# Kernel optimization log

Hardware: AMD Instinct MI355X
Metric: run time of the kernel (lower is better)

The kernel has to match this reference:

```python
import jax, jax.numpy as jnp
import numpy as np

B, S, HID = 4, 4096, 1024
H, D = 16, 64  # num_head, attn_dim
EPS = 1e-6


def setup_inputs() -> dict:
    key = jax.random.key(0)
    ks = jax.random.split(key, 9)
    sc = 1.0 / np.sqrt(HID)
    return {
        "x": jax.random.normal(ks[0], (B, S, HID), jnp.float32),
        "Wq": jax.random.normal(ks[1], (HID, H * D), jnp.float32) * sc,
        "bq": jnp.zeros((H * D,), jnp.float32),
        "Wk": jax.random.normal(ks[2], (HID, H * D), jnp.float32) * sc,
        "bk": jnp.zeros((H * D,), jnp.float32),
        "Wv": jax.random.normal(ks[3], (HID, H * D), jnp.float32) * sc,
        "bv": jnp.zeros((H * D,), jnp.float32),
        "Wo": jax.random.normal(ks[4], (H * D, HID), jnp.float32) * sc,
        "bo": jnp.zeros((HID,), jnp.float32),
    }


def _phi(x):
    # feature_map == 'elu': elu(x) + 1
    return jax.nn.elu(x) + 1.0


def reference(x, Wq, bq, Wk, bk, Wv, bv, Wo, bo):
    bs, n, _ = x.shape
    # projections -> [b, n, h, d], then scan axis first -> [n, b, h, d]
    Q = _phi((x @ Wq + bq).reshape(bs, n, H, D)).transpose(1, 0, 2, 3)
    K = _phi((x @ Wk + bk).reshape(bs, n, H, D)).transpose(1, 0, 2, 3)
    V = (x @ Wv + bv).reshape(bs, n, H, D).transpose(1, 0, 2, 3)

    KV0 = jnp.zeros((bs, H, D, D), x.dtype)
    Ks0 = jnp.zeros((bs, H, D), x.dtype)

    def step(carry, qkv):
        KV, Ks = carry
        qi, ki, vi = qkv  # each [b, h, d]
        KV = KV + jnp.einsum('bhd,bhe->bhde', ki, vi)
        Ks = Ks + ki
        num = jnp.einsum('bhd,bhde->bhe', qi, KV)
        den = jnp.einsum('bhd,bhd->bh', qi, Ks)
        return (KV, Ks), num / (den[..., None] + EPS)

    _, out = jax.lax.scan(step, (KV0, Ks0), (Q, K, V))  # out: [n, b, h, d]
    out = out.transpose(1, 0, 2, 3).reshape(bs, n, H * D)
    return out @ Wo + bo
```

## Files before the change

### kernel.cpp

```cpp
#include <hip/hip_runtime.h>
#include <stdint.h>


#define DEVI __device__ __forceinline__

typedef __attribute__((ext_vector_type(8))) short bf16x8;
typedef __attribute__((ext_vector_type(4))) float f32x4;
typedef unsigned short u16;

DEVI u16 f2bf(float f) {
  union { float f; uint32_t u; } x; x.f = f;
  return (u16)((x.u + 0x7FFFu + ((x.u >> 16) & 1u)) >> 16);
}
DEVI float bf2f(u16 u) {
  union { uint32_t u; float f; } x; x.u = ((uint32_t)u) << 16;
  return x.f;
}
DEVI f32x4 mfma16(bf16x8 a, bf16x8 b, f32x4 c) {
  return __builtin_amdgcn_mfma_f32_16x16x32_bf16(a, b, c, 0, 0, 0);
}

typedef __attribute__((address_space(3))) void* lds_vp;
typedef const __attribute__((address_space(1))) void* glb_vp;
DEVI void gload_lds16(const void* g, void* l) {
  __builtin_amdgcn_global_load_lds((glb_vp)g, (lds_vp)l, 16, 0, 0);
}

#define BAR()   asm volatile("s_barrier" ::: "memory")
#define LGKM0() do { asm volatile("s_waitcnt lgkmcnt(0)" ::: "memory"); \
                     __builtin_amdgcn_sched_barrier(0); } while (0)

static constexpr int Ss  = 4096;
static constexpr int Hh  = 16;
static constexpr int CC  = 64;
static constexpr int NCC = Ss / CC;

__global__ __launch_bounds__(256) void cvt_bf16_k(const float* __restrict__ in,
                                                  u16* __restrict__ out, int n8) {
  const int i = blockIdx.x * 256 + threadIdx.x;
  if (i >= n8) return;
  const float4* p = (const float4*)(in + (size_t)i * 8);
  const float4 a = p[0], b = p[1];
  union { uint4 v; u16 s[8]; } u;
  u.s[0] = f2bf(a.x); u.s[1] = f2bf(a.y); u.s[2] = f2bf(a.z); u.s[3] = f2bf(a.w);
  u.s[4] = f2bf(b.x); u.s[5] = f2bf(b.y); u.s[6] = f2bf(b.z); u.s[7] = f2bf(b.w);
  ((uint4*)out)[i] = u.v;
}

__global__ __launch_bounds__(256) void transpose_cvt4_k(const float* __restrict__ w0,
                                                        const float* __restrict__ w1,
                                                        const float* __restrict__ w2,
                                                        const float* __restrict__ w3,
                                                        u16* __restrict__ dqkv,
                                                        u16* __restrict__ dwo) {
  __shared__ float tl[32][33];
  const int z = blockIdx.z;
  const float* in = (z == 0) ? w0 : (z == 1) ? w1 : (z == 2) ? w2 : w3;
  u16* out = (z < 3) ? (dqkv + (size_t)z * 1024 * 1024) : dwo;
  const int tx = threadIdx.x & 31, ty = threadIdx.x >> 5;
  const int bx = blockIdx.x, by = blockIdx.y;
#pragma unroll
  for (int j = 0; j < 4; ++j)
    tl[ty + j * 8][tx] = in[(size_t)(by * 32 + ty + j * 8) * 1024 + bx * 32 + tx];
  __syncthreads();
#pragma unroll
  for (int j = 0; j < 4; ++j)
    out[(size_t)(bx * 32 + ty + j * 8) * 1024 + by * 32 + tx] = f2bf(tl[tx][ty + j * 8]);
}

template <bool FUSED, bool OUTF32>
__global__ __launch_bounds__(512, 2) void gemm256_k(const u16* __restrict__ A,
                                                    const u16* __restrict__ BT,
                                                    const float* __restrict__ b0,
                                                    const float* __restrict__ b1,
                                                    const float* __restrict__ b2,
                                                    void* __restrict__ out,
                                                    int M, int K) {
  __shared__ __attribute__((aligned(16))) u16 lds[65536];
  const int t = threadIdx.x, lane = t & 63, w = t >> 6;
  const int wm = w >> 2, wn = w & 3;

  const int nx = gridDim.x;
  const int nwg = nx * gridDim.y;
  const int bid = blockIdx.y * nx + blockIdx.x;
  const int swz = (bid & 7) * (nwg >> 3) + (bid >> 3);
  const int bx = swz % nx, by = swz / nx;
  const int m0 = by * 256, n0 = bx * 256;

  const u16* gA = A + (size_t)m0 * K;
  const u16* gB = BT + (size_t)n0 * K;

  const int sr = t >> 2;
  const int sc = (t & 3) ^ ((sr >> 1) & 3);
  auto stage = [&](const u16* gm, u16* dst, int kof) {
    gload_lds16(gm + (size_t)sr * K + kof + sc * 8, dst + t * 8);
    gload_lds16(gm + (size_t)(sr + 128) * K + kof + sc * 8, dst + 4096 + t * 8);
  };

  f32x4 acc[8][4];
#pragma unroll
  for (int i = 0; i < 8; ++i)
#pragma unroll
    for (int j = 0; j < 4; ++j) acc[i][j] = f32x4{0.f, 0.f, 0.f, 0.f};

  stage(gA, lds, 0);          stage(gB, lds + 32768, 0);
  stage(gA, lds + 8192, 32);  stage(gB, lds + 40960, 32);
  asm volatile("s_waitcnt vmcnt(4)" ::: "memory");
  BAR();

  const int fr = lane & 15, kq = lane >> 4;
  const int rdko = ((kq ^ ((fr >> 1) & 3)) << 3);
  const int arow0 = wm * 128 + fr;
  const int brow0 = wn * 64 + fr;

  const int nk = K >> 6;
  for (int kt = 0; kt < nk; ++kt) {
    const int d = kt & 1;
    const bool pf = (kt + 1 < nk);
    const int kon = (kt + 1) << 6;
    u16* Ac = lds + d * 16384;
    u16* Bc = lds + 32768 + d * 16384;
    u16* An = lds + (d ^ 1) * 16384;
    u16* Bn = lds + 32768 + (d ^ 1) * 16384;
    bf16x8 af[8], bg0, bg1;
#pragma unroll
    for (int h = 0; h < 2; ++h) {
      const u16* Ah = Ac + h * 8192;
      const u16* Bh = Bc + h * 8192;
#pragma unroll
      for (int fi = 0; fi < 8; ++fi)
        af[fi] = *(const bf16x8*)(Ah + (arow0 + fi * 16) * 32 + rdko);
      bg0 = *(const bf16x8*)(Bh + brow0 * 32 + rdko);
      bg1 = *(const bf16x8*)(Bh + (brow0 + 16) * 32 + rdko);
      if (pf) stage(gA, An + h * 8192, kon + h * 32);
      BAR();
      LGKM0();
      __builtin_amdgcn_s_setprio(1);
#pragma unroll
      for (int fi = 0; fi < 8; ++fi) {
        acc[fi][0] = mfma16(af[fi], bg0, acc[fi][0]);
        acc[fi][1] = mfma16(af[fi], bg1, acc[fi][1]);
      }
      __builtin_amdgcn_s_setprio(0);
      __builtin_amdgcn_sched_barrier(0);
      BAR();
      bg0 = *(const bf16x8*)(Bh + (brow0 + 32) * 32 + rdko);
      bg1 = *(const bf16x8*)(Bh + (brow0 + 48) * 32 + rdko);
      if (pf) stage(gB, Bn + h * 8192, kon + h * 32);
      BAR();
      LGKM0();
      __builtin_amdgcn_s_setprio(1);
#pragma unroll
      for (int fi = 0; fi < 8; ++fi) {
        acc[fi][2] = mfma16(af[fi], bg0, acc[fi][2]);
        acc[fi][3] = mfma16(af[fi], bg1, acc[fi][3]);
      }
      __builtin_amdgcn_s_setprio(0);
      __builtin_amdgcn_sched_barrier(0);
      if (h == 0) {
        if (pf) asm volatile("s_waitcnt vmcnt(4)" ::: "memory");
        else    asm volatile("s_waitcnt vmcnt(0)" ::: "memory");
      } else if (pf) {
        asm volatile("s_waitcnt vmcnt(4)" ::: "memory");
      }
      BAR();
    }
  }

  const int rowg = (lane >> 4) * 4;
  if constexpr (!OUTF32) {
    __syncthreads();
    const int seg  = FUSED ? (n0 >> 10) : 0;
    const int lcol0 = FUSED ? (n0 & 1023) : n0;
    const float* bp = b0;
    if constexpr (FUSED) bp = (seg == 0) ? b0 : (seg == 1) ? b1 : b2;
#pragma unroll
    for (int fj = 0; fj < 4; ++fj) {
      const int col = wn * 64 + fj * 16 + fr;
      const float bv = bp[lcol0 + col];
#pragma unroll
      for (int fi = 0; fi < 8; ++fi) {
#pragma unroll
        for (int rr = 0; rr < 4; ++rr) {
          const int row = wm * 128 + fi * 16 + rowg + rr;
          float v = acc[fi][fj][rr] + bv;
          if (FUSED && seg < 2) v = (v > 0.f) ? (v + 1.f) : __expf(v);
          lds[row * 256 + (((col >> 3) ^ ((row >> 2) & 31)) << 3) + (col & 7)] = f2bf(v);
        }
      }
    }
    __syncthreads();
    u16* outp = (u16*)out + (size_t)seg * M * 1024 + (size_t)m0 * 1024 + lcol0;
#pragma unroll
    for (int it = 0; it < 16; ++it) {
      const int g = it * 512 + t;
      const int row = g >> 5, c16 = g & 31;
      const uint4 v = *(const uint4*)&lds[row * 256 + ((c16 ^ ((row >> 2) & 31)) << 3)];
      *(uint4*)(outp + (size_t)row * 1024 + c16 * 8) = v;
    }
  } else {
    float* flds = (float*)lds;
#pragma unroll
    for (int pass = 0; pass < 2; ++pass) {
      __syncthreads();
      if (wm == pass) {
#pragma unroll
        for (int fj = 0; fj < 4; ++fj) {
          const int col = wn * 64 + fj * 16 + fr;
          const float bv = b0[n0 + col];
#pragma unroll
          for (int fi = 0; fi < 8; ++fi) {
#pragma unroll
            for (int rr = 0; rr < 4; ++rr) {
              const int rl = fi * 16 + rowg + rr;
              flds[rl * 256 + (((col >> 2) ^ ((rl >> 2) & 63)) << 2) + (col & 3)] =
                  acc[fi][fj][rr] + bv;
            }
          }
        }
      }
      __syncthreads();
      float* outp = (float*)out + (size_t)(m0 + pass * 128) * 1024 + n0;
#pragma unroll
      for (int it = 0; it < 16; ++it) {
        const int g = it * 512 + t;
        const int row = g >> 6, c16 = g & 63;
        const uint4 v = *(const uint4*)&flds[row * 256 + ((c16 ^ ((row >> 2) & 63)) << 2)];
        *(uint4*)(outp + (size_t)row * 1024 + c16 * 4) = v;
      }
    }
  }
}

__global__ __launch_bounds__(256) void chunk_kv_k(const u16* __restrict__ Kb,
                                                  const u16* __restrict__ Vb,
                                                  u16* __restrict__ KVTc,
                                                  float* __restrict__ Ksc) {
  const int c = blockIdx.x, h = blockIdx.y, b = blockIdx.z;
  __shared__ u16 KT[64][72], VT[64][72];
  const int t = threadIdx.x, lane = t & 63, w = t >> 6;
  {
    const int i = t >> 2, c0 = (t & 3) * 16;
    const size_t g = ((size_t)(b * Ss + c * CC + i)) * 1024 + h * 64 + c0;
    const u16* kp = Kb + g;
    const u16* vp = Vb + g;
#pragma unroll
    for (int j = 0; j < 16; ++j) { KT[c0 + j][i] = kp[j]; VT[c0 + j][i] = vp[j]; }
  }
  __syncthreads();
  f32x4 acc[4];
#pragma unroll
  for (int j = 0; j < 4; ++j) acc[j] = f32x4{0.f, 0.f, 0.f, 0.f};
  const int fr = lane & 15, kq = (lane >> 4) * 8;
#pragma unroll
  for (int kk = 0; kk < 2; ++kk) {
    const bf16x8 av = *(const bf16x8*)&VT[w * 16 + fr][kk * 32 + kq];
#pragma unroll
    for (int fj = 0; fj < 4; ++fj) {
      const bf16x8 bk = *(const bf16x8*)&KT[fj * 16 + fr][kk * 32 + kq];
      acc[fj] = mfma16(av, bk, acc[fj]);
    }
  }
  const size_t base = ((size_t)((b * Hh + h) * NCC + c)) * 4096;
#pragma unroll
  for (int fj = 0; fj < 4; ++fj)
#pragma unroll
    for (int rr = 0; rr < 4; ++rr) {
      const int e = w * 16 + (lane >> 4) * 4 + rr;
      const int d = fj * 16 + fr;
      KVTc[base + (size_t)e * 64 + d] = f2bf(acc[fj][rr]);
    }
  if (t < 64) {
    float s = 0.f;
#pragma unroll
    for (int ii = 0; ii < 8; ++ii) {
      const bf16x8 kv = *(const bf16x8*)&KT[t][ii * 8];
#pragma unroll
      for (int j = 0; j < 8; ++j) s += bf2f((u16)kv[j]);
    }
    Ksc[((size_t)((b * Hh + h) * NCC + c)) * 64 + t] = s;
  }
}

__global__ __launch_bounds__(256) void prefix_k(const u16* __restrict__ KVTc,
                                                const float* __restrict__ Ksc,
                                                u16* __restrict__ KVpreT,
                                                float* __restrict__ Kspre) {
  const int bh = blockIdx.x, eg = blockIdx.y;
  const int t = threadIdx.x;
  const int e4 = eg * 1024 + t * 4;
  const u16* src = KVTc + (size_t)bh * NCC * 4096 + e4;
  u16* dst = KVpreT + (size_t)bh * NCC * 4096 + e4;
  const float* kss = Ksc + (size_t)bh * NCC * 64 + t;
  float* ksd = Kspre + (size_t)bh * NCC * 64 + t;
  float run[4] = {0.f, 0.f, 0.f, 0.f};
  float rk = 0.f;
  for (int c = 0; c < NCC; ++c) {
    union { uint2 v; u16 s[4]; } in, ov;
    in.v = *(const uint2*)(src + (size_t)c * 4096);
#pragma unroll
    for (int j = 0; j < 4; ++j) { ov.s[j] = f2bf(run[j]); run[j] += bf2f(in.s[j]); }
    *(uint2*)(dst + (size_t)c * 4096) = ov.v;
    if (eg == 0 && t < 64) { ksd[(size_t)c * 64] = rk; rk += kss[(size_t)c * 64]; }
  }
}

__global__ __launch_bounds__(256) void chunk_out_k(const u16* __restrict__ Qb,
                                                   const u16* __restrict__ Kb,
                                                   const u16* __restrict__ Vb,
                                                   const u16* __restrict__ KVpreT,
                                                   const float* __restrict__ Kspre,
                                                   u16* __restrict__ attn) {
  const int c = blockIdx.x, h = blockIdx.y, b = blockIdx.z;
  const int bh = b * Hh + h;
  __shared__ u16 Ql[64][72], Kl[64][72], VT[64][72], Pl[64][72];
  __shared__ float den[64];
  const int t = threadIdx.x, lane = t & 63, w = t >> 6;

  {
    const int i = t >> 2, c0 = (t & 3) * 16;
    const size_t g = ((size_t)(b * Ss + c * CC + i)) * 1024 + h * 64 + c0;
    const uint4* qp = (const uint4*)(Qb + g);
    uint4* qd = (uint4*)&Ql[i][c0]; qd[0] = qp[0]; qd[1] = qp[1];
    const uint4* kp = (const uint4*)(Kb + g);
    uint4* kd = (uint4*)&Kl[i][c0]; kd[0] = kp[0]; kd[1] = kp[1];
    const u16* vp = Vb + g;
#pragma unroll
    for (int j = 0; j < 16; ++j) VT[c0 + j][i] = vp[j];
  }
  __syncthreads();

  f32x4 sacc[4];
#pragma unroll
  for (int fj = 0; fj < 4; ++fj) sacc[fj] = f32x4{0.f, 0.f, 0.f, 0.f};
#pragma unroll
  for (int kd = 0; kd < 2; ++kd) {
    const bf16x8 aq = *(const bf16x8*)&Ql[w * 16 + (lane & 15)][kd * 32 + (lane >> 4) * 8];
#pragma unroll
    for (int fj = 0; fj < 4; ++fj) {
      const bf16x8 bk = *(const bf16x8*)&Kl[fj * 16 + (lane & 15)][kd * 32 + (lane >> 4) * 8];
      sacc[fj] = mfma16(aq, bk, sacc[fj]);
    }
  }
  float rowsum[4] = {0.f, 0.f, 0.f, 0.f};
#pragma unroll
  for (int fj = 0; fj < 4; ++fj) {
#pragma unroll
    for (int rr = 0; rr < 4; ++rr) {
      const int i_loc = w * 16 + (lane >> 4) * 4 + rr;
      const int j_loc = fj * 16 + (lane & 15);
      const float v = (j_loc <= i_loc) ? sacc[fj][rr] : 0.f;
      Pl[i_loc][j_loc] = f2bf(v);
      rowsum[rr] += v;
    }
  }
#pragma unroll
  for (int off = 1; off < 16; off <<= 1) {
#pragma unroll
    for (int rr = 0; rr < 4; ++rr) rowsum[rr] += __shfl_xor(rowsum[rr], off, 64);
  }
  if ((lane & 15) == 0) {
#pragma unroll
    for (int rr = 0; rr < 4; ++rr) den[w * 16 + (lane >> 4) * 4 + rr] = rowsum[rr];
  }
  __syncthreads();
  {
    const int i = t >> 2, part = t & 3;
    const float* ksp = Kspre + ((size_t)(bh * NCC + c)) * 64 + part * 16;
    float s = 0.f;
#pragma unroll
    for (int sg = 0; sg < 2; ++sg) {
      const bf16x8 q = *(const bf16x8*)&Ql[i][part * 16 + sg * 8];
#pragma unroll
      for (int j = 0; j < 8; ++j) s += bf2f((u16)q[j]) * ksp[sg * 8 + j];
    }
    s += __shfl_xor(s, 1, 64);
    s += __shfl_xor(s, 2, 64);
    if (part == 0) den[i] = den[i] + s + 1e-6f;
  }
  __syncthreads();

  f32x4 oacc[4];
#pragma unroll
  for (int fj = 0; fj < 4; ++fj) oacc[fj] = f32x4{0.f, 0.f, 0.f, 0.f};
  const u16* kvb = KVpreT + ((size_t)(bh * NCC + c)) * 4096;
#pragma unroll
  for (int ks2 = 0; ks2 < 2; ++ks2) {
    const bf16x8 aq = *(const bf16x8*)&Ql[w * 16 + (lane & 15)][ks2 * 32 + (lane >> 4) * 8];
#pragma unroll
    for (int fj = 0; fj < 4; ++fj) {
      const bf16x8 bv =
          *(const bf16x8*)(kvb + (size_t)(fj * 16 + (lane & 15)) * 64 + ks2 * 32 + (lane >> 4) * 8);
      oacc[fj] = mfma16(aq, bv, oacc[fj]);
    }
  }
#pragma unroll
  for (int ks3 = 0; ks3 < 2; ++ks3) {
    const bf16x8 ap = *(const bf16x8*)&Pl[w * 16 + (lane & 15)][ks3 * 32 + (lane >> 4) * 8];
#pragma unroll
    for (int fj = 0; fj < 4; ++fj) {
      const bf16x8 bv = *(const bf16x8*)&VT[fj * 16 + (lane & 15)][ks3 * 32 + (lane >> 4) * 8];
      oacc[fj] = mfma16(ap, bv, oacc[fj]);
    }
  }
#pragma unroll
  for (int fj = 0; fj < 4; ++fj) {
#pragma unroll
    for (int rr = 0; rr < 4; ++rr) {
      const int i_loc = w * 16 + (lane >> 4) * 4 + rr;
      const int e = fj * 16 + (lane & 15);
      const float v = oacc[fj][rr] / den[i_loc];
      attn[((size_t)(b * Ss + c * CC + i_loc)) * 1024 + h * 64 + e] = f2bf(v);
    }
  }
}

extern "C" void kernel_launch(void* const* d_in, const int* in_sizes, int n_in,
                              void* d_out, int out_size, void* d_ws, size_t ws_size,
                              hipStream_t stream) {
  (void)in_sizes; (void)n_in; (void)out_size; (void)ws_size;
  const float* x  = (const float*)d_in[0];
  const float* Wq = (const float*)d_in[1];
  const float* bq = (const float*)d_in[2];
  const float* Wk = (const float*)d_in[3];
  const float* bk = (const float*)d_in[4];
  const float* Wv = (const float*)d_in[5];
  const float* bv = (const float*)d_in[6];
  const float* Wo = (const float*)d_in[7];
  const float* bo = (const float*)d_in[8];
  float* out = (float*)d_out;
  char* ws = (char*)d_ws;

  size_t off = 0;
  auto take = [&](size_t bytes) { size_t r = off; off += (bytes + 255) & ~(size_t)255; return r; };
  const size_t WQKV_B = (size_t)3072 * 1024 * 2;
  const size_t WT_B   = (size_t)1024 * 1024 * 2;
  const size_t BIG_B  = (size_t)16384 * 1024 * 2;
  const size_t KVT_B  = (size_t)64 * NCC * 4096 * 2;
  const size_t KS_B   = (size_t)64 * NCC * 64 * 4;

  u16* WqkvT  = (u16*)(ws + take(WQKV_B));
  u16* WoT    = (u16*)(ws + take(WT_B));
  size_t shared_off = take(BIG_B);
  u16* xbf    = (u16*)(ws + shared_off);
  u16* KVTc   = (u16*)(ws + shared_off);
  u16* attn   = (u16*)(ws + shared_off);
  u16* Qb     = (u16*)(ws + take(BIG_B));
  u16* Kb     = (u16*)(ws + take(BIG_B));
  u16* Vb     = (u16*)(ws + take(BIG_B));
  u16* KVpreT = (u16*)(ws + take(KVT_B));
  float* Ksc  = (float*)(ws + take(KS_B));
  float* Kspre= (float*)(ws + take(KS_B));

  const dim3 blk(256);
  cvt_bf16_k<<<dim3(8192), blk, 0, stream>>>(x, xbf, 16384 * 1024 / 8);
  transpose_cvt4_k<<<dim3(32, 32, 4), blk, 0, stream>>>(Wq, Wk, Wv, Wo, WqkvT, WoT);

  gemm256_k<true, false><<<dim3(12, 64), dim3(512), 0, stream>>>(
      xbf, WqkvT, bq, bk, bv, Qb, 16384, 1024);

  const dim3 gC(NCC, Hh, 4);
  chunk_kv_k<<<gC, blk, 0, stream>>>(Kb, Vb, KVTc, Ksc);
  prefix_k<<<dim3(64, 4), blk, 0, stream>>>(KVTc, Ksc, KVpreT, Kspre);
  chunk_out_k<<<gC, blk, 0, stream>>>(Qb, Kb, Vb, KVpreT, Kspre, attn);

  gemm256_k<false, true><<<dim3(4, 64), dim3(512), 0, stream>>>(
      attn, WoT, bo, NULL, NULL, out, 16384, 1024);
}
```

Before: 266.3 us.

## Switch GEMM main loop to triple-buffered 32-wide K tiles with smaller LDS

The 256x256 GEMM mainloop goes from double-buffered 64-wide K stages to a three-slot ring of 32-wide K stages prefetched two steps ahead. This shrinks shared memory from 128KB to 96KB. The epilogues are reorganised into more passes so they fit in the smaller LDS. The aim is deeper load latency hiding and lower LDS use, at the cost of more barriers per unit of K work and extra epilogue passes.

After: 275.5 us. 1.03x slower.

```diff
diff --git a/kernel.cpp b/kernel.cpp
--- a/kernel.cpp
+++ b/kernel.cpp
@@ -76,7 +76,7 @@
                                                     const float* __restrict__ b2,
                                                     void* __restrict__ out,
                                                     int M, int K) {
-  __shared__ __attribute__((aligned(16))) u16 lds[65536];
+  __shared__ __attribute__((aligned(16))) u16 lds[49152];
   const int t = threadIdx.x, lane = t & 63, w = t >> 6;
   const int wm = w >> 2, wn = w & 3;
 
@@ -103,103 +103,74 @@
 #pragma unroll
     for (int j = 0; j < 4; ++j) acc[i][j] = f32x4{0.f, 0.f, 0.f, 0.f};
 
-  stage(gA, lds, 0);          stage(gB, lds + 32768, 0);
-  stage(gA, lds + 8192, 32);  stage(gB, lds + 40960, 32);
-  asm volatile("s_waitcnt vmcnt(4)" ::: "memory");
-  BAR();
+  stage(gA, lds, 0);          stage(gB, lds + 24576, 0);
+  stage(gA, lds + 8192, 32);  stage(gB, lds + 24576 + 8192, 32);
 
   const int fr = lane & 15, kq = lane >> 4;
   const int rdko = ((kq ^ ((fr >> 1) & 3)) << 3);
   const int arow0 = wm * 128 + fr;
   const int brow0 = wn * 64 + fr;
 
-  const int nk = K >> 6;
+  const int nk = K >> 5;
+  int cb = 0;
   for (int kt = 0; kt < nk; ++kt) {
-    const int d = kt & 1;
-    const bool pf = (kt + 1 < nk);
-    const int kon = (kt + 1) << 6;
-    u16* Ac = lds + d * 16384;
-    u16* Bc = lds + 32768 + d * 16384;
-    u16* An = lds + (d ^ 1) * 16384;
-    u16* Bn = lds + 32768 + (d ^ 1) * 16384;
-    bf16x8 af[8], bg0, bg1;
-#pragma unroll
-    for (int h = 0; h < 2; ++h) {
-      const u16* Ah = Ac + h * 8192;
-      const u16* Bh = Bc + h * 8192;
-#pragma unroll
-      for (int fi = 0; fi < 8; ++fi)
-        af[fi] = *(const bf16x8*)(Ah + (arow0 + fi * 16) * 32 + rdko);
-      bg0 = *(const bf16x8*)(Bh + brow0 * 32 + rdko);
-      bg1 = *(const bf16x8*)(Bh + (brow0 + 16) * 32 + rdko);
-      if (pf) stage(gA, An + h * 8192, kon + h * 32);
-      BAR();
-      LGKM0();
-      __builtin_amdgcn_s_setprio(1);
-#pragma unroll
-      for (int fi = 0; fi < 8; ++fi) {
-        acc[fi][0] = mfma16(af[fi], bg0, acc[fi][0]);
-        acc[fi][1] = mfma16(af[fi], bg1, acc[fi][1]);
-      }
-      __builtin_amdgcn_s_setprio(0);
-      __builtin_amdgcn_sched_barrier(0);
-      BAR();
-      bg0 = *(const bf16x8*)(Bh + (brow0 + 32) * 32 + rdko);
-      bg1 = *(const bf16x8*)(Bh + (brow0 + 48) * 32 + rdko);
-      if (pf) stage(gB, Bn + h * 8192, kon + h * 32);
-      BAR();
-      LGKM0();
-      __builtin_amdgcn_s_setprio(1);
-#pragma unroll
-      for (int fi = 0; fi < 8; ++fi) {
-        acc[fi][2] = mfma16(af[fi], bg0, acc[fi][2]);
-        acc[fi][3] = mfma16(af[fi], bg1, acc[fi][3]);
-      }
-      __builtin_amdgcn_s_setprio(0);
-      __builtin_amdgcn_sched_barrier(0);
-      if (h == 0) {
-        if (pf) asm volatile("s_waitcnt vmcnt(4)" ::: "memory");
-        else    asm volatile("s_waitcnt vmcnt(0)" ::: "memory");
-      } else if (pf) {
-        asm volatile("s_waitcnt vmcnt(4)" ::: "memory");
-      }
-      BAR();
-    }
+    int nb = cb + 2; if (nb >= 3) nb -= 3;
+    const u16* Ac = lds + cb * 8192;
+    const u16* Bc = lds + 24576 + cb * 8192;
+    u16* An = lds + nb * 8192;
+    u16* Bn = lds + 24576 + nb * 8192;
+    const bool pf = (kt + 2 < nk);
+    const int kon = (kt + 2) << 5;
+
+    if (kt + 1 < nk) asm volatile("s_waitcnt vmcnt(4)" ::: "memory");
+    else             asm volatile("s_waitcnt vmcnt(0)" ::: "memory");
+    BAR();
+
+    bf16x8 a0[4], bg[4];
+#pragma unroll
+    for (int fi = 0; fi < 4; ++fi)
+      a0[fi] = *(const bf16x8*)(Ac + (arow0 + fi * 16) * 32 + rdko);
+#pragma unroll
+    for (int fj = 0; fj < 4; ++fj)
+      bg[fj] = *(const bf16x8*)(Bc + (brow0 + fj * 16) * 32 + rdko);
+    if (pf) stage(gA, An, kon);
+    BAR();
+    LGKM0();
+    __builtin_amdgcn_s_setprio(1);
+#pragma unroll
+    for (int fi = 0; fi < 4; ++fi)
+#pragma unroll
+      for (int fj = 0; fj < 4; ++fj)
+        acc[fi][fj] = mfma16(a0[fi], bg[fj], acc[fi][fj]);
+    __builtin_amdgcn_s_setprio(0);
+    __builtin_amdgcn_sched_barrier(0);
+    BAR();
+
+    bf16x8 a1[4];
+#pragma unroll
+    for (int fi = 0; fi < 4; ++fi)
+      a1[fi] = *(const bf16x8*)(Ac + (arow0 + 64 + fi * 16) * 32 + rdko);
+    if (pf) stage(gB, Bn, kon);
+    BAR();
+    LGKM0();
+    __builtin_amdgcn_s_setprio(1);
+#pragma unroll
+    for (int fi = 0; fi < 4; ++fi)
+#pragma unroll
+      for (int fj = 0; fj < 4; ++fj)
+        acc[4 + fi][fj] = mfma16(a1[fi], bg[fj], acc[4 + fi][fj]);
+    __builtin_amdgcn_s_setprio(0);
+    __builtin_amdgcn_sched_barrier(0);
+    cb = (cb + 1 == 3) ? 0 : cb + 1;
   }
 
   const int rowg = (lane >> 4) * 4;
   if constexpr (!OUTF32) {
-    __syncthreads();
-    const int seg  = FUSED ? (n0 >> 10) : 0;
+    const int seg   = FUSED ? (n0 >> 10) : 0;
     const int lcol0 = FUSED ? (n0 & 1023) : n0;
     const float* bp = b0;
     if constexpr (FUSED) bp = (seg == 0) ? b0 : (seg == 1) ? b1 : b2;
-#pragma unroll
-    for (int fj = 0; fj < 4; ++fj) {
-      const int col = wn * 64 + fj * 16 + fr;
-      const float bv = bp[lcol0 + col];
-#pragma unroll
-      for (int fi = 0; fi < 8; ++fi) {
-#pragma unroll
-        for (int rr = 0; rr < 4; ++rr) {
-          const int row = wm * 128 + fi * 16 + rowg + rr;
-          float v = acc[fi][fj][rr] + bv;
-          if (FUSED && seg < 2) v = (v > 0.f) ? (v + 1.f) : __expf(v);
-          lds[row * 256 + (((col >> 3) ^ ((row >> 2) & 31)) << 3) + (col & 7)] = f2bf(v);
-        }
-      }
-    }
-    __syncthreads();
     u16* outp = (u16*)out + (size_t)seg * M * 1024 + (size_t)m0 * 1024 + lcol0;
-#pragma unroll
-    for (int it = 0; it < 16; ++it) {
-      const int g = it * 512 + t;
-      const int row = g >> 5, c16 = g & 31;
-      const uint4 v = *(const uint4*)&lds[row * 256 + ((c16 ^ ((row >> 2) & 31)) << 3)];
-      *(uint4*)(outp + (size_t)row * 1024 + c16 * 8) = v;
-    }
-  } else {
-    float* flds = (float*)lds;
 #pragma unroll
     for (int pass = 0; pass < 2; ++pass) {
       __syncthreads();
@@ -207,12 +178,44 @@
 #pragma unroll
         for (int fj = 0; fj < 4; ++fj) {
           const int col = wn * 64 + fj * 16 + fr;
-          const float bv = b0[n0 + col];
+          const float bv = bp[lcol0 + col];
 #pragma unroll
           for (int fi = 0; fi < 8; ++fi) {
 #pragma unroll
             for (int rr = 0; rr < 4; ++rr) {
               const int rl = fi * 16 + rowg + rr;
+              float v = acc[fi][fj][rr] + bv;
+              if (FUSED && seg < 2) v = (v > 0.f) ? (v + 1.f) : __expf(v);
+              lds[rl * 256 + (((col >> 3) ^ ((rl >> 2) & 31)) << 3) + (col & 7)] = f2bf(v);
+            }
+          }
+        }
+      }
+      __syncthreads();
+#pragma unroll
+      for (int it = 0; it < 8; ++it) {
+        const int g = it * 512 + t;
+        const int row = g >> 5, c16 = g & 31;
+        const uint4 v = *(const uint4*)&lds[row * 256 + ((c16 ^ ((row >> 2) & 31)) << 3)];
+        *(uint4*)(outp + (size_t)(pass * 128 + row) * 1024 + c16 * 8) = v;
+      }
+    }
+  } else {
+    float* flds = (float*)lds;
+#pragma unroll
+    for (int pass = 0; pass < 4; ++pass) {
+      __syncthreads();
+      if (wm == (pass >> 1)) {
+#pragma unroll
+        for (int fj = 0; fj < 4; ++fj) {
+          const int col = wn * 64 + fj * 16 + fr;
+          const float bv = b0[n0 + col];
+#pragma unroll
+          for (int fi2 = 0; fi2 < 4; ++fi2) {
+            const int fi = (pass & 1) * 4 + fi2;
+#pragma unroll
+            for (int rr = 0; rr < 4; ++rr) {
+              const int rl = fi2 * 16 + rowg + rr;
               flds[rl * 256 + (((col >> 2) ^ ((rl >> 2) & 63)) << 2) + (col & 3)] =
                   acc[fi][fj][rr] + bv;
             }
@@ -220,13 +223,12 @@
         }
       }
       __syncthreads();
-      float* outp = (float*)out + (size_t)(m0 + pass * 128) * 1024 + n0;
-#pragma unroll
-      for (int it = 0; it < 16; ++it) {
+#pragma unroll
+      for (int it = 0; it < 8; ++it) {
         const int g = it * 512 + t;
         const int row = g >> 6, c16 = g & 63;
         const uint4 v = *(const uint4*)&flds[row * 256 + ((c16 ^ ((row >> 2) & 63)) << 2)];
-        *(uint4*)(outp + (size_t)row * 1024 + c16 * 4) = v;
+        *(uint4*)((float*)out + (size_t)(m0 + pass * 64 + row) * 1024 + n0 + c16 * 4) = v;
       }
     }
   }
```
